# Optimization experiments

Measured on AMD Instinct MI355X. Metric: run time of the kernel, lower is better.

## Reference

```python
import jax, jax.numpy as jnp
import numpy as np

N_CELLS = 1000          # cells in minibatch
N_GENES_OI = 500        # genes in minibatch
N_GENES_TOTAL = 5000    # fragments.n_genes
N_LATENT = 10           # latent (cluster) dim
NBINS = 128             # quadratic spline bins
N_KNOTS = NBINS + 1     # knot heights = mixture delta components
N_CUTS = 1_000_000      # fragment cut sites (ragged dim)


def setup_inputs() -> dict:
    key = jax.random.key(0)
    ks = jax.random.split(key, 10)
    return {
        "latent": jax.random.normal(ks[0], (N_CELLS, N_LATENT), jnp.float32),
        "cut_coordinates": jax.random.uniform(ks[1], (N_CUTS,), jnp.float32),
        "genes_oi": jax.random.randint(ks[2], (N_GENES_OI,), 0, N_GENES_TOTAL),
        "cut_local_cellxgene_ix": jax.random.randint(ks[3], (N_CUTS,), 0, N_CELLS * N_GENES_OI),
        "cut_localcellxgene_ix": jax.random.randint(ks[4], (N_CUTS,), 0, N_CELLS * N_GENES_TOTAL),
        "cut_local_gene_ix": jax.random.randint(ks[5], (N_CUTS,), 0, N_GENES_OI),
        "height_slope_w": jax.random.normal(ks[6], (N_GENES_TOTAL, N_LATENT, N_KNOTS), jnp.float32) * 0.1,
        "overall_slope_w": jax.random.normal(ks[7], (N_GENES_TOTAL, N_LATENT), jnp.float32) * 0.1,
        "overall_baseline": jax.random.normal(ks[8], (N_GENES_TOTAL,), jnp.float32),
        "spline_baseline": jax.random.normal(ks[9], (N_GENES_TOTAL, N_KNOTS), jnp.float32) * 0.5,
    }


def quadratic_spline_log_prob(x, heights):
    """Piecewise-linear density (quadratic CDF spline) with K equal-width bins.
    heights: [ncuts, K+1] unnormalized log knot heights; x in [0,1]."""
    K = heights.shape[-1] - 1
    h = heights - jnp.max(heights, axis=-1, keepdims=True)  # stable; pdf invariant to shift
    u = jnp.exp(h)
    # trapezoid integral with width 1/K
    norm = jnp.sum(0.5 * (u[:, :-1] + u[:, 1:]), axis=-1) / K
    pdf = u / norm[:, None]                                 # [ncuts, K+1]
    xs = jnp.clip(x, 0.0, 1.0 - 1e-6) * K
    b = jnp.clip(jnp.floor(xs).astype(jnp.int32), 0, K - 1)  # bin index
    alpha = xs - b
    left = jnp.take_along_axis(pdf, b[:, None], axis=1)[:, 0]
    right = jnp.take_along_axis(pdf, (b + 1)[:, None], axis=1)[:, 0]
    return jnp.log(left + alpha * (right - left))


def reference(latent, cut_coordinates, genes_oi, cut_local_cellxgene_ix,
              cut_localcellxgene_ix, cut_local_gene_ix, height_slope_w,
              overall_slope_w, overall_baseline, spline_baseline):
    # decoder: per-gene slope embeddings modulated by cell latent
    height_delta = jnp.einsum('cl,glk->cgk', latent, height_slope_w[genes_oi])  # [N, Goi, K+1]
    overall_delta = latent @ overall_slope_w.T                                  # [N, G]
    # softmax over all genes -> per cell x gene overall rate
    overall_cellxgene = jax.nn.softmax(overall_baseline[None, :] + overall_delta, axis=-1)
    # ragged gathers per cut
    overall = overall_cellxgene.reshape(-1)[cut_localcellxgene_ix]              # [ncuts]
    height = height_delta.reshape(-1, height_delta.shape[-1])[cut_local_cellxgene_ix]  # [ncuts, K+1]
    gene_per_cut = genes_oi[cut_local_gene_ix]
    heights = spline_baseline[gene_per_cut] + height                            # [ncuts, K+1]
    likelihood_height = quadratic_spline_log_prob(cut_coordinates, heights)
    likelihood = likelihood_height + jnp.log(overall) + jnp.log(jnp.float32(N_GENES_TOTAL))
    elbo = -jnp.sum(likelihood)
    return elbo
```

## Files before the change

### kernel.cpp

```cpp
#include <hip/hip_runtime.h>
#include <hip/hip_fp16.h>

#define N_CELLS   1000
#define N_GOI     500
#define N_GTOT    5000
#define N_LAT     10
#define NBINS     128
#define N_KNOTS   129
#define LOG_NGT   8.517193191416238f
#define LOG_NBINS 4.852030263919617f
#define LSE_CPB   4
#define OVB       20

typedef int   vint4   __attribute__((ext_vector_type(4)));
typedef float vfloat4 __attribute__((ext_vector_type(4)));
typedef float vfloat2 __attribute__((ext_vector_type(2)));

#if defined(__has_builtin)
#if __has_builtin(__builtin_amdgcn_cvt_pk_f32_fp8) && \
    __has_builtin(__builtin_amdgcn_cvt_pk_fp8_f32)
#define HW_FP8 1
#endif
#endif

#ifdef HW_FP8
#define DEC2(w, hi) ((vfloat2)__builtin_amdgcn_cvt_pk_f32_fp8((int)(w), (hi)))
__device__ __forceinline__ unsigned enc1(float x) {
    return (unsigned)__builtin_amdgcn_cvt_pk_fp8_f32(x, x, 0, false) & 0xffu;
}
#else
__device__ __forceinline__ float dec1_sw(unsigned b) {
    unsigned s = b >> 7, e = (b >> 3) & 15, m = b & 7;
    float v = (e == 0) ? ldexpf((float)m, -9)
                       : ldexpf((float)(8 + m), (int)e - 10);
    return s ? -v : v;
}
__device__ __forceinline__ vfloat2 dec2_sw(unsigned w, int hi) {
    unsigned sh = hi ? 16u : 0u;
    vfloat2 r;
    r.x = dec1_sw((w >> sh) & 0xffu);
    r.y = dec1_sw((w >> (sh + 8)) & 0xffu);
    return r;
}
#define DEC2(w, hi) dec2_sw((w), (hi))
__device__ __forceinline__ unsigned enc1(float x) {
    unsigned s = (__float_as_uint(x) >> 31) << 7;
    float ax = fabsf(x);
    if (!(ax > 0.0f)) return s;
    ax = fminf(ax, 448.0f);
    int e; frexpf(ax, &e);
    int qe = (e - 1 < -6) ? -9 : e - 4;
    float rq = ldexpf(rintf(ldexpf(ax, -qe)), qe);
    if (rq == 0.0f) return s;
    frexpf(rq, &e);
    int be = e - 1 + 7;
    if (be <= 0) return s | (unsigned)rintf(ldexpf(rq, 9));
    unsigned mm = (unsigned)rintf(ldexpf(rq, -(e - 1)) * 8.0f);
    return s | ((unsigned)be << 3) | (mm - 8u);
}
#endif

__device__ __forceinline__ float2 upk(unsigned u) {
    union { unsigned u; __half2 h; } cv; cv.u = u;
    return __half22float2(cv.h);
}
__device__ __forceinline__ float dec1(unsigned b) {
    return DEC2(b, false).x;
}


__global__ __launch_bounds__(256) void prep_pair_kernel(
    const float* __restrict__ latent,
    const float* __restrict__ osw,
    const float* __restrict__ ob,
    const int*  __restrict__ genes_oi,
    const float* __restrict__ hsw,
    const float* __restrict__ sbase,
    __half* __restrict__ latph,
    uint4*  __restrict__ wpair,
    uint4*  __restrict__ ovp8,
    signed char* __restrict__ lnsq,
    float* __restrict__ out)
{
    const int t = threadIdx.x;
    __shared__ float          wq[N_KNOTS * 12];
    __shared__ unsigned char  bq[N_KNOTS * 10];
    __shared__ unsigned short hq[N_KNOTS];
    __shared__ float          wred[4][4];

    if (blockIdx.x < N_GOI) {
        const int gi = blockIdx.x;
        const int g  = genes_oi[gi];
        for (int e = t; e < N_KNOTS * 12; e += 256) {
            const int k = e / 12;
            const int l = e - 12 * k;
            float v = 0.0f;
            if (l < N_LAT) {
                const unsigned b8 = enc1(hsw[(g * N_LAT + l) * N_KNOTS + k]);
                bq[k * 10 + l] = (unsigned char)b8;
                v = dec1(b8);
            } else if (l == N_LAT) {
                const __half h = __float2half(sbase[g * N_KNOTS + k]);
                hq[k] = __half_as_ushort(h);
                v = __half2float(h);
            }
            wq[e] = v;
        }
        __syncthreads();

        {
            const int b  = t >> 1;
            const int hf = t & 1;
            const int row = b + hf;
            const unsigned char* bb = bq + row * 10;
            uint4 rec;
            rec.x = (unsigned)bb[0] | ((unsigned)bb[1] << 8) |
                    ((unsigned)bb[2] << 16) | ((unsigned)bb[3] << 24);
            rec.y = (unsigned)bb[4] | ((unsigned)bb[5] << 8) |
                    ((unsigned)bb[6] << 16) | ((unsigned)bb[7] << 24);
            rec.z = (unsigned)bb[8] | ((unsigned)bb[9] << 8) |
                    ((unsigned)hq[row] << 16);
            rec.w = 0u;
            wpair[(gi * 128 + b) * 2 + hf] = rec;
        }

        float lat[4][N_LAT];
#pragma unroll
        for (int j = 0; j < 4; ++j) {
            const int cj = t + j * 256;
            const int c  = cj < N_CELLS ? cj : 0;
            const float2* l2 = (const float2*)(latent + c * N_LAT);
#pragma unroll
            for (int h = 0; h < 5; ++h) {
                const float2 v2 = l2[h];
                lat[j][2 * h]     = v2.x;
                lat[j][2 * h + 1] = v2.y;
            }
        }
        float sum[4] = {0.f, 0.f, 0.f, 0.f};
#pragma unroll 2
        for (int k = 0; k <= NBINS; ++k) {
            const float tw = (k == 0 || k == NBINS) ? 0.5f : 1.0f;
            const float4* wr = (const float4*)(wq + k * 12);
            const float4 wa = wr[0], wb = wr[1], wc = wr[2];
#pragma unroll
            for (int j = 0; j < 4; ++j) {
                float d = wc.z;
                d = fmaf(lat[j][0], wa.x, d); d = fmaf(lat[j][1], wa.y, d);
                d = fmaf(lat[j][2], wa.z, d); d = fmaf(lat[j][3], wa.w, d);
                d = fmaf(lat[j][4], wb.x, d); d = fmaf(lat[j][5], wb.y, d);
                d = fmaf(lat[j][6], wb.z, d); d = fmaf(lat[j][7], wb.w, d);
                d = fmaf(lat[j][8], wc.x, d); d = fmaf(lat[j][9], wc.y, d);
                sum[j] += tw * __expf(d);
            }
        }
#pragma unroll
        for (int j = 0; j < 4; ++j) {
            const int c = t + j * 256;
            if (c < N_CELLS) {
                const float lns = __logf(sum[j]) - LOG_NBINS;
                const float qv = fminf(fmaxf(lns * 32.0f, -127.0f), 127.0f);
                lnsq[gi * N_CELLS + c] = (signed char)(int)rintf(qv);
            }
        }
    } else if (blockIdx.x < N_GOI + (N_CELLS / LSE_CPB)) {
        const int cb = (blockIdx.x - N_GOI) * LSE_CPB;
        float lat[LSE_CPB][N_LAT];
#pragma unroll
        for (int j = 0; j < LSE_CPB; ++j) {
            const float2* l2 = (const float2*)(latent + (cb + j) * N_LAT);
#pragma unroll
            for (int h = 0; h < 5; ++h) {
                const float2 v2 = l2[h];
                lat[j][2 * h]     = v2.x;
                lat[j][2 * h + 1] = v2.y;
            }
        }
        float s[LSE_CPB] = {0.f, 0.f, 0.f, 0.f};
        for (int g = t; g < N_GTOT; g += 256) {
            const float bb = ob[g];
            const float2* o2 = (const float2*)(osw + g * N_LAT);
            float2 w0 = o2[0], w1 = o2[1], w2 = o2[2], w3 = o2[3], w4 = o2[4];
#pragma unroll
            for (int j = 0; j < LSE_CPB; ++j) {
                float v = bb;
                v = fmaf(lat[j][0], w0.x, v); v = fmaf(lat[j][1], w0.y, v);
                v = fmaf(lat[j][2], w1.x, v); v = fmaf(lat[j][3], w1.y, v);
                v = fmaf(lat[j][4], w2.x, v); v = fmaf(lat[j][5], w2.y, v);
                v = fmaf(lat[j][6], w3.x, v); v = fmaf(lat[j][7], w3.y, v);
                v = fmaf(lat[j][8], w4.x, v); v = fmaf(lat[j][9], w4.y, v);
                s[j] += __expf(v);
            }
        }
#pragma unroll
        for (int j = 0; j < LSE_CPB; ++j)
#pragma unroll
            for (int off = 32; off; off >>= 1) s[j] += __shfl_xor(s[j], off);
        if ((t & 63) == 0)
#pragma unroll
            for (int j = 0; j < LSE_CPB; ++j) wred[t >> 6][j] = s[j];
        __syncthreads();
        if (t < 16 * LSE_CPB) {
            const int j = t >> 4;
            const int l = t & 15;
            const float bias = LOG_NGT -
                __logf(wred[0][j] + wred[1][j] + wred[2][j] + wred[3][j]);
            float v = 0.0f;
            if (l < N_LAT)       v = latent[(cb + j) * N_LAT + l];
            else if (l == N_LAT) v = 1.0f;
            else if (l == 11)    v = bias;
            latph[(cb + j) * 16 + l] = __float2half(v);
        }
    } else {
        const int vb = blockIdx.x - N_GOI - (N_CELLS / LSE_CPB);
        for (int g = vb * 256 + t; g < N_GTOT; g += OVB * 256) {
            const float* o = osw + g * N_LAT;
            uint4 rec;
            rec.x = enc1(o[0]) | (enc1(o[1]) << 8) |
                    (enc1(o[2]) << 16) | (enc1(o[3]) << 24);
            rec.y = enc1(o[4]) | (enc1(o[5]) << 8) |
                    (enc1(o[6]) << 16) | (enc1(o[7]) << 24);
            rec.z = enc1(o[8]) | (enc1(o[9]) << 8) |
                    ((unsigned)__half_as_ushort(__float2half(ob[g])) << 16);
            rec.w = 0u;
            ovp8[g] = rec;
        }
        if (vb == 0 && t == 0) *out = 0.0f;
    }
}

__device__ __forceinline__ float cut_term(
    int pi, int qi, float x,
    const __half* __restrict__ lsh,
    const uint4*  __restrict__ wpair,
    const uint4*  __restrict__ ovp8,
    const signed char* __restrict__ lnsq)
{
    const unsigned p    = (unsigned)pi;
    const unsigned cell = p / (unsigned)N_GOI;
    const unsigned gl   = p - cell * (unsigned)N_GOI;
    const unsigned q    = (unsigned)qi;
    const unsigned c2   = q / (unsigned)N_GTOT;
    const unsigned g2   = q - c2 * (unsigned)N_GTOT;

    float xs = fminf(fmaxf(x, 0.0f), 1.0f - 1e-6f) * (float)NBINS;
    int b = (int)xs;
    b = b < NBINS - 1 ? b : NBINS - 1;
    const float alpha = xs - (float)b;

    const uint4 r0 = wpair[((gl << 7) + b) * 2];
    const uint4 r1 = wpair[((gl << 7) + b) * 2 + 1];
    const uint4 ov = ovp8[g2];
    const float lns = (float)lnsq[gl * (unsigned)N_CELLS + cell] * 0.03125f;

    const __half* lc = lsh + (cell << 4);
    const uint4 lca = *(const uint4*)(lc);
    const unsigned lcb = *(const unsigned*)(lc + 8);
    const __half* mc = lsh + (c2 << 4);
    const uint4 mca = *(const uint4*)(mc);
    const uint2 mcb = *(const uint2*)(mc + 8);

    const float2 a0 = upk(lca.x), a1 = upk(lca.y), a2 = upk(lca.z),
                 a3 = upk(lca.w), a4 = upk(lcb);

    vfloat2 w01 = DEC2(r0.x, false), w23 = DEC2(r0.x, true),
            w45 = DEC2(r0.y, false), w67 = DEC2(r0.y, true),
            w89 = DEC2(r0.z, false);
    float d0 = upk(r0.z).y;
    d0 = fmaf(a0.x, w01.x, d0); d0 = fmaf(a0.y, w01.y, d0);
    d0 = fmaf(a1.x, w23.x, d0); d0 = fmaf(a1.y, w23.y, d0);
    d0 = fmaf(a2.x, w45.x, d0); d0 = fmaf(a2.y, w45.y, d0);
    d0 = fmaf(a3.x, w67.x, d0); d0 = fmaf(a3.y, w67.y, d0);
    d0 = fmaf(a4.x, w89.x, d0); d0 = fmaf(a4.y, w89.y, d0);

    vfloat2 v01 = DEC2(r1.x, false), v23 = DEC2(r1.x, true),
            v45 = DEC2(r1.y, false), v67 = DEC2(r1.y, true),
            v89 = DEC2(r1.z, false);
    float d1 = upk(r1.z).y;
    d1 = fmaf(a0.x, v01.x, d1); d1 = fmaf(a0.y, v01.y, d1);
    d1 = fmaf(a1.x, v23.x, d1); d1 = fmaf(a1.y, v23.y, d1);
    d1 = fmaf(a2.x, v45.x, d1); d1 = fmaf(a2.y, v45.y, d1);
    d1 = fmaf(a3.x, v67.x, d1); d1 = fmaf(a3.y, v67.y, d1);
    d1 = fmaf(a4.x, v89.x, d1); d1 = fmaf(a4.y, v89.y, d1);

    const float ul = __expf(d0);
    const float ur = __expf(d1);
    const float pv = fmaf(alpha, ur - ul, ul);

    const float2 m0 = upk(mca.x), m1 = upk(mca.y), m2 = upk(mca.z),
                 m3 = upk(mca.w), m4 = upk(mcb.x), mb = upk(mcb.y);
    vfloat2 o01 = DEC2(ov.x, false), o23 = DEC2(ov.x, true),
            o45 = DEC2(ov.y, false), o67 = DEC2(ov.y, true),
            o89 = DEC2(ov.z, false);
    float dv = upk(ov.z).y + mb.y;
    dv = fmaf(m0.x, o01.x, dv); dv = fmaf(m0.y, o01.y, dv);
    dv = fmaf(m1.x, o23.x, dv); dv = fmaf(m1.y, o23.y, dv);
    dv = fmaf(m2.x, o45.x, dv); dv = fmaf(m2.y, o45.y, dv);
    dv = fmaf(m3.x, o67.x, dv); dv = fmaf(m3.y, o67.y, dv);
    dv = fmaf(m4.x, o89.x, dv); dv = fmaf(m4.y, o89.y, dv);

    return __logf(pv) - lns + dv;
}

__global__ __launch_bounds__(256, 2) void cut_kernel(
    const __half* __restrict__ latph,
    const uint4*  __restrict__ wpair,
    const uint4*  __restrict__ ovp8,
    const signed char* __restrict__ lnsq,
    const float* __restrict__ coords,
    const int*  __restrict__ cxg,
    const int*  __restrict__ cxgtot,
    float* __restrict__ out, int n)
{
    const int t = threadIdx.x;
    __shared__ __half lsh[N_CELLS * 16];
    {
        const uint4* s = (const uint4*)latph;
        uint4* d = (uint4*)lsh;
        for (int e = t; e < (N_CELLS * 16) / 8; e += 256) d[e] = s[e];
    }
    __syncthreads();

    double acc = 0.0;
    const int i0 = (blockIdx.x * 256 + t) * 4;
    if (i0 + 3 < n) {
        const vint4   P = __builtin_nontemporal_load((const vint4*)(cxg + i0));
        const vint4   Q = __builtin_nontemporal_load((const vint4*)(cxgtot + i0));
        const vfloat4 X = __builtin_nontemporal_load((const vfloat4*)(coords + i0));
        acc += (double)cut_term(P.x, Q.x, X.x, lsh, wpair, ovp8, lnsq);
        acc += (double)cut_term(P.y, Q.y, X.y, lsh, wpair, ovp8, lnsq);
        acc += (double)cut_term(P.z, Q.z, X.z, lsh, wpair, ovp8, lnsq);
        acc += (double)cut_term(P.w, Q.w, X.w, lsh, wpair, ovp8, lnsq);
    } else {
        for (int i = i0; i < n; ++i)
            acc += (double)cut_term(cxg[i], cxgtot[i], coords[i],
                                    lsh, wpair, ovp8, lnsq);
    }

#pragma unroll
    for (int off = 32; off; off >>= 1) acc += __shfl_xor(acc, off);
    __shared__ double part[4];
    if ((t & 63) == 0) part[t >> 6] = acc;
    __syncthreads();
    if (t == 0)
        atomicAdd(out, (float)(-(part[0] + part[1] + part[2] + part[3])));
}

extern "C" void kernel_launch(void* const* d_in, const int* in_sizes, int n_in,
                              void* d_out, int out_size, void* d_ws, size_t ws_size,
                              hipStream_t stream)
{
    const float* latent   = (const float*)d_in[0];
    const float* coords   = (const float*)d_in[1];
    const int*   genes_oi = (const int*)  d_in[2];
    const int*   cxg      = (const int*)  d_in[3];
    const int*   cxg_tot  = (const int*)  d_in[4];
    const float* hsw      = (const float*)d_in[6];
    const float* osw      = (const float*)d_in[7];
    const float* ob       = (const float*)d_in[8];
    const float* sbase    = (const float*)d_in[9];
    const int ncuts = in_sizes[1];

    char* ws = (char*)d_ws;
    __half* latph = (__half*)(ws);
    uint4*  wpair = (uint4*) (ws + 32000);
    uint4*  ovp8  = (uint4*) (ws + 2080000);
    signed char* lnsq = (signed char*)(ws + 2160000);
    float*  out   = (float*)d_out;

    prep_pair_kernel<<<N_GOI + (N_CELLS / LSE_CPB) + OVB, 256, 0, stream>>>(
        latent, osw, ob, genes_oi, hsw, sbase,
        latph, wpair, ovp8, lnsq, out);

    const int nq = (ncuts + 3) >> 2;
    const int blocks = (nq + 255) >> 8;
    cut_kernel<<<blocks, 256, 0, stream>>>(
        latph, wpair, ovp8, lnsq, coords, cxg, cxg_tot, out, ncuts);
}
```

Baseline: 149.9 us.

## Split prep kernel, use packed fp16 FMA for normalizers, widen cuts per thread

The fused prep kernel is split into a per-gene kernel and a per-cell/overall kernel. The per-gene kernel now computes the spline normalizer dot products with packed half2 FMAs on fp16 latents and weights, which halves the FMA count, but the logits are accumulated in half precision and lose accuracy. The cut kernel processes 8 cuts per thread instead of 4 and drops the occupancy hint from launch bounds, giving more memory-level parallelism per thread at the cost of more registers. The extra launch adds a little overhead.

```diff
diff --git a/kernel.cpp b/kernel.cpp
--- a/kernel.cpp
+++ b/kernel.cpp
@@ -11,6 +11,7 @@
 #define LOG_NBINS 4.852030263919617f
 #define LSE_CPB   4
 #define OVB       20
+#define CUTS_PT   8
 
 typedef int   vint4   __attribute__((ext_vector_type(4)));
 typedef float vfloat4 __attribute__((ext_vector_type(4)));
@@ -64,107 +65,136 @@
     union { unsigned u; __half2 h; } cv; cv.u = u;
     return __half22float2(cv.h);
 }
-__device__ __forceinline__ float dec1(unsigned b) {
-    return DEC2(b, false).x;
-}
-
-
-__global__ __launch_bounds__(256) void prep_pair_kernel(
+__device__ __forceinline__ __half2 h2(unsigned u) {
+    union { unsigned u; __half2 h; } cv; cv.u = u;
+    return cv.h;
+}
+__device__ __forceinline__ float dec1(unsigned b) { return DEC2(b, false).x; }
+
+
+__global__ __launch_bounds__(256) void prep_gene_kernel(
+    const float* __restrict__ latent,
+    const int*  __restrict__ genes_oi,
+    const float* __restrict__ hsw,
+    const float* __restrict__ sbase,
+    uint4*  __restrict__ wpair,
+    signed char* __restrict__ lnsq)
+{
+    const int t  = threadIdx.x;
+    const int gi = blockIdx.x;
+    const int g  = genes_oi[gi];
+
+    __shared__ uint4          wdup4[N_KNOTS * 3];
+    __shared__ unsigned char  bq[N_KNOTS * 10];
+    __shared__ unsigned short hq[N_KNOTS];
+
+    {
+        unsigned* wd = (unsigned*)wdup4;
+        for (int e = t; e < N_KNOTS * 12; e += 256) {
+            const int k = e / 12;
+            const int l = e - 12 * k;
+            unsigned dup = 0u;
+            if (l < N_LAT) {
+                const unsigned b8 = enc1(hsw[(g * N_LAT + l) * N_KNOTS + k]);
+                bq[k * 10 + l] = (unsigned char)b8;
+                const unsigned hb =
+                    (unsigned)__half_as_ushort(__float2half(dec1(b8)));
+                dup = hb | (hb << 16);
+            } else if (l == N_LAT) {
+                const __half h = __float2half(sbase[g * N_KNOTS + k]);
+                hq[k] = __half_as_ushort(h);
+                const unsigned hb = (unsigned)__half_as_ushort(h);
+                dup = hb | (hb << 16);
+            }
+            wd[e] = dup;
+        }
+    }
+    __syncthreads();
+
+    {
+        const int b   = t >> 1;
+        const int hf  = t & 1;
+        const int row = b + hf;
+        const unsigned char* bb = bq + row * 10;
+        uint4 rec;
+        rec.x = (unsigned)bb[0] | ((unsigned)bb[1] << 8) |
+                ((unsigned)bb[2] << 16) | ((unsigned)bb[3] << 24);
+        rec.y = (unsigned)bb[4] | ((unsigned)bb[5] << 8) |
+                ((unsigned)bb[6] << 16) | ((unsigned)bb[7] << 24);
+        rec.z = (unsigned)bb[8] | ((unsigned)bb[9] << 8) |
+                ((unsigned)hq[row] << 16);
+        rec.w = 0u;
+        wpair[(gi * 128 + b) * 2 + hf] = rec;
+    }
+
+    __half2 lA[N_LAT], lB[N_LAT];
+    {
+        const int cA0 = t;
+        const int cA1 = t + 256;
+        const int cB0 = t + 512;
+        const int cB1 = (t + 768 < N_CELLS) ? t + 768 : 0;
+#pragma unroll
+        for (int l = 0; l < N_LAT; ++l) {
+            lA[l] = __halves2half2(__float2half(latent[cA0 * N_LAT + l]),
+                                   __float2half(latent[cA1 * N_LAT + l]));
+            lB[l] = __halves2half2(__float2half(latent[cB0 * N_LAT + l]),
+                                   __float2half(latent[cB1 * N_LAT + l]));
+        }
+    }
+
+    float s0 = 0.f, s1 = 0.f, s2 = 0.f, s3 = 0.f;
+#pragma unroll 2
+    for (int k = 0; k <= NBINS; ++k) {
+        const float tw = (k == 0 || k == NBINS) ? 0.5f : 1.0f;
+        const uint4 a = wdup4[k * 3];
+        const uint4 b = wdup4[k * 3 + 1];
+        const uint4 c = wdup4[k * 3 + 2];
+        __half2 dA = h2(c.z), dB = h2(c.z);
+        dA = __hfma2(lA[0], h2(a.x), dA); dB = __hfma2(lB[0], h2(a.x), dB);
+        dA = __hfma2(lA[1], h2(a.y), dA); dB = __hfma2(lB[1], h2(a.y), dB);
+        dA = __hfma2(lA[2], h2(a.z), dA); dB = __hfma2(lB[2], h2(a.z), dB);
+        dA = __hfma2(lA[3], h2(a.w), dA); dB = __hfma2(lB[3], h2(a.w), dB);
+        dA = __hfma2(lA[4], h2(b.x), dA); dB = __hfma2(lB[4], h2(b.x), dB);
+        dA = __hfma2(lA[5], h2(b.y), dA); dB = __hfma2(lB[5], h2(b.y), dB);
+        dA = __hfma2(lA[6], h2(b.z), dA); dB = __hfma2(lB[6], h2(b.z), dB);
+        dA = __hfma2(lA[7], h2(b.w), dA); dB = __hfma2(lB[7], h2(b.w), dB);
+        dA = __hfma2(lA[8], h2(c.x), dA); dB = __hfma2(lB[8], h2(c.x), dB);
+        dA = __hfma2(lA[9], h2(c.y), dA); dB = __hfma2(lB[9], h2(c.y), dB);
+        const float2 fA = __half22float2(dA);
+        const float2 fB = __half22float2(dB);
+        s0 += tw * __expf(fA.x);
+        s1 += tw * __expf(fA.y);
+        s2 += tw * __expf(fB.x);
+        s3 += tw * __expf(fB.y);
+    }
+
+    {
+        float sums[4] = {s0, s1, s2, s3};
+#pragma unroll
+        for (int j = 0; j < 4; ++j) {
+            const int c = t + j * 256;
+            if (c < N_CELLS) {
+                const float lns = __logf(sums[j]) - LOG_NBINS;
+                const float qv = fminf(fmaxf(lns * 32.0f, -127.0f), 127.0f);
+                lnsq[gi * N_CELLS + c] = (signed char)(int)rintf(qv);
+            }
+        }
+    }
+}
+
+__global__ __launch_bounds__(256) void prep_cell_kernel(
     const float* __restrict__ latent,
     const float* __restrict__ osw,
     const float* __restrict__ ob,
-    const int*  __restrict__ genes_oi,
-    const float* __restrict__ hsw,
-    const float* __restrict__ sbase,
     __half* __restrict__ latph,
-    uint4*  __restrict__ wpair,
     uint4*  __restrict__ ovp8,
-    signed char* __restrict__ lnsq,
     float* __restrict__ out)
 {
     const int t = threadIdx.x;
-    __shared__ float          wq[N_KNOTS * 12];
-    __shared__ unsigned char  bq[N_KNOTS * 10];
-    __shared__ unsigned short hq[N_KNOTS];
-    __shared__ float          wred[4][4];
-
-    if (blockIdx.x < N_GOI) {
-        const int gi = blockIdx.x;
-        const int g  = genes_oi[gi];
-        for (int e = t; e < N_KNOTS * 12; e += 256) {
-            const int k = e / 12;
-            const int l = e - 12 * k;
-            float v = 0.0f;
-            if (l < N_LAT) {
-                const unsigned b8 = enc1(hsw[(g * N_LAT + l) * N_KNOTS + k]);
-                bq[k * 10 + l] = (unsigned char)b8;
-                v = dec1(b8);
-            } else if (l == N_LAT) {
-                const __half h = __float2half(sbase[g * N_KNOTS + k]);
-                hq[k] = __half_as_ushort(h);
-                v = __half2float(h);
-            }
-            wq[e] = v;
-        }
-        __syncthreads();
-
-        {
-            const int b  = t >> 1;
-            const int hf = t & 1;
-            const int row = b + hf;
-            const unsigned char* bb = bq + row * 10;
-            uint4 rec;
-            rec.x = (unsigned)bb[0] | ((unsigned)bb[1] << 8) |
-                    ((unsigned)bb[2] << 16) | ((unsigned)bb[3] << 24);
-            rec.y = (unsigned)bb[4] | ((unsigned)bb[5] << 8) |
-                    ((unsigned)bb[6] << 16) | ((unsigned)bb[7] << 24);
-            rec.z = (unsigned)bb[8] | ((unsigned)bb[9] << 8) |
-                    ((unsigned)hq[row] << 16);
-            rec.w = 0u;
-            wpair[(gi * 128 + b) * 2 + hf] = rec;
-        }
-
-        float lat[4][N_LAT];
-#pragma unroll
-        for (int j = 0; j < 4; ++j) {
-            const int cj = t + j * 256;
-            const int c  = cj < N_CELLS ? cj : 0;
-            const float2* l2 = (const float2*)(latent + c * N_LAT);
-#pragma unroll
-            for (int h = 0; h < 5; ++h) {
-                const float2 v2 = l2[h];
-                lat[j][2 * h]     = v2.x;
-                lat[j][2 * h + 1] = v2.y;
-            }
-        }
-        float sum[4] = {0.f, 0.f, 0.f, 0.f};
-#pragma unroll 2
-        for (int k = 0; k <= NBINS; ++k) {
-            const float tw = (k == 0 || k == NBINS) ? 0.5f : 1.0f;
-            const float4* wr = (const float4*)(wq + k * 12);
-            const float4 wa = wr[0], wb = wr[1], wc = wr[2];
-#pragma unroll
-            for (int j = 0; j < 4; ++j) {
-                float d = wc.z;
-                d = fmaf(lat[j][0], wa.x, d); d = fmaf(lat[j][1], wa.y, d);
-                d = fmaf(lat[j][2], wa.z, d); d = fmaf(lat[j][3], wa.w, d);
-                d = fmaf(lat[j][4], wb.x, d); d = fmaf(lat[j][5], wb.y, d);
-                d = fmaf(lat[j][6], wb.z, d); d = fmaf(lat[j][7], wb.w, d);
-                d = fmaf(lat[j][8], wc.x, d); d = fmaf(lat[j][9], wc.y, d);
-                sum[j] += tw * __expf(d);
-            }
-        }
-#pragma unroll
-        for (int j = 0; j < 4; ++j) {
-            const int c = t + j * 256;
-            if (c < N_CELLS) {
-                const float lns = __logf(sum[j]) - LOG_NBINS;
-                const float qv = fminf(fmaxf(lns * 32.0f, -127.0f), 127.0f);
-                lnsq[gi * N_CELLS + c] = (signed char)(int)rintf(qv);
-            }
-        }
-    } else if (blockIdx.x < N_GOI + (N_CELLS / LSE_CPB)) {
-        const int cb = (blockIdx.x - N_GOI) * LSE_CPB;
+    __shared__ float wred[4][LSE_CPB];
+
+    if (blockIdx.x < N_CELLS / LSE_CPB) {
+        const int cb = blockIdx.x * LSE_CPB;
         float lat[LSE_CPB][N_LAT];
 #pragma unroll
         for (int j = 0; j < LSE_CPB; ++j) {
@@ -212,7 +242,7 @@
             latph[(cb + j) * 16 + l] = __float2half(v);
         }
     } else {
-        const int vb = blockIdx.x - N_GOI - (N_CELLS / LSE_CPB);
+        const int vb = blockIdx.x - N_CELLS / LSE_CPB;
         for (int g = vb * 256 + t; g < N_GTOT; g += OVB * 256) {
             const float* o = osw + g * N_LAT;
             uint4 rec;
@@ -302,7 +332,7 @@
     return __logf(pv) - lns + dv;
 }
 
-__global__ __launch_bounds__(256, 2) void cut_kernel(
+__global__ __launch_bounds__(256) void cut_kernel(
     const __half* __restrict__ latph,
     const uint4*  __restrict__ wpair,
     const uint4*  __restrict__ ovp8,
@@ -322,15 +352,22 @@
     __syncthreads();
 
     double acc = 0.0;
-    const int i0 = (blockIdx.x * 256 + t) * 4;
-    if (i0 + 3 < n) {
-        const vint4   P = __builtin_nontemporal_load((const vint4*)(cxg + i0));
-        const vint4   Q = __builtin_nontemporal_load((const vint4*)(cxgtot + i0));
-        const vfloat4 X = __builtin_nontemporal_load((const vfloat4*)(coords + i0));
-        acc += (double)cut_term(P.x, Q.x, X.x, lsh, wpair, ovp8, lnsq);
-        acc += (double)cut_term(P.y, Q.y, X.y, lsh, wpair, ovp8, lnsq);
-        acc += (double)cut_term(P.z, Q.z, X.z, lsh, wpair, ovp8, lnsq);
-        acc += (double)cut_term(P.w, Q.w, X.w, lsh, wpair, ovp8, lnsq);
+    const int i0 = (blockIdx.x * 256 + t) * CUTS_PT;
+    if (i0 + CUTS_PT - 1 < n) {
+        const vint4   Pa = __builtin_nontemporal_load((const vint4*)(cxg + i0));
+        const vint4   Pb = __builtin_nontemporal_load((const vint4*)(cxg + i0 + 4));
+        const vint4   Qa = __builtin_nontemporal_load((const vint4*)(cxgtot + i0));
+        const vint4   Qb = __builtin_nontemporal_load((const vint4*)(cxgtot + i0 + 4));
+        const vfloat4 Xa = __builtin_nontemporal_load((const vfloat4*)(coords + i0));
+        const vfloat4 Xb = __builtin_nontemporal_load((const vfloat4*)(coords + i0 + 4));
+        acc += (double)cut_term(Pa.x, Qa.x, Xa.x, lsh, wpair, ovp8, lnsq);
+        acc += (double)cut_term(Pa.y, Qa.y, Xa.y, lsh, wpair, ovp8, lnsq);
+        acc += (double)cut_term(Pa.z, Qa.z, Xa.z, lsh, wpair, ovp8, lnsq);
+        acc += (double)cut_term(Pa.w, Qa.w, Xa.w, lsh, wpair, ovp8, lnsq);
+        acc += (double)cut_term(Pb.x, Qb.x, Xb.x, lsh, wpair, ovp8, lnsq);
+        acc += (double)cut_term(Pb.y, Qb.y, Xb.y, lsh, wpair, ovp8, lnsq);
+        acc += (double)cut_term(Pb.z, Qb.z, Xb.z, lsh, wpair, ovp8, lnsq);
+        acc += (double)cut_term(Pb.w, Qb.w, Xb.w, lsh, wpair, ovp8, lnsq);
     } else {
         for (int i = i0; i < n; ++i)
             acc += (double)cut_term(cxg[i], cxgtot[i], coords[i],
@@ -368,11 +405,12 @@
     signed char* lnsq = (signed char*)(ws + 2160000);
     float*  out   = (float*)d_out;
 
-    prep_pair_kernel<<<N_GOI + (N_CELLS / LSE_CPB) + OVB, 256, 0, stream>>>(
-        latent, osw, ob, genes_oi, hsw, sbase,
-        latph, wpair, ovp8, lnsq, out);
-
-    const int nq = (ncuts + 3) >> 2;
+    prep_gene_kernel<<<N_GOI, 256, 0, stream>>>(
+        latent, genes_oi, hsw, sbase, wpair, lnsq);
+    prep_cell_kernel<<<N_CELLS / LSE_CPB + OVB, 256, 0, stream>>>(
+        latent, osw, ob, latph, ovp8, out);
+
+    const int nq = (ncuts + CUTS_PT - 1) / CUTS_PT;
     const int blocks = (nq + 255) >> 8;
     cut_kernel<<<blocks, 256, 0, stream>>>(
         latph, wpair, ovp8, lnsq, coords, cxg, cxg_tot, out, ncuts);
```

New measurement: 156.1 us. 4.1% more time.
